# Optimization experiments

Measured on AMD Instinct MI355X. Metric: run time of the kernel, lower is better.

## Reference

```python
import jax, jax.numpy as jnp
import numpy as np

D_MODEL = 1024
NUM_HEAD = 16
HEAD_DIM = D_MODEL // NUM_HEAD
D_OUT = 1024
B, S = 2, 2048


def setup_inputs() -> dict:
    key = jax.random.key(0)
    ks = jax.random.split(key, 11)
    s = 0.02
    return {
        "Q": jax.random.normal(ks[0], (B, S, D_MODEL), jnp.float32),
        "K": jax.random.normal(ks[1], (B, S, D_MODEL), jnp.float32),
        "V": jax.random.normal(ks[2], (B, S, D_MODEL), jnp.float32),
        "Wq": jax.random.normal(ks[3], (D_MODEL, D_MODEL), jnp.float32) * s,
        "bq": jnp.zeros((D_MODEL,), jnp.float32),
        "Wk": jax.random.normal(ks[4], (D_MODEL, D_MODEL), jnp.float32) * s,
        "bk": jnp.zeros((D_MODEL,), jnp.float32),
        "Wv": jax.random.normal(ks[5], (D_MODEL, D_MODEL), jnp.float32) * s,
        "bv": jnp.zeros((D_MODEL,), jnp.float32),
        "Wo": jax.random.normal(ks[6], (D_MODEL, D_OUT), jnp.float32) * s,
        "bo": jnp.zeros((D_OUT,), jnp.float32),
    }


def reference(Q, K, V, Wq, bq, Wk, bk, Wv, bv, Wo, bo):
    T = jnp.asarray(HEAD_DIM, Q.dtype) ** 0.5
    b = Q.shape[0]
    q = (Q @ Wq + bq) / T                      # [B,S,D]
    k = K @ Wk + bk
    v = V @ Wv + bv
    q = q.reshape(b, -1, NUM_HEAD, HEAD_DIM)   # [B,S,H,d]
    k = k.reshape(b, -1, NUM_HEAD, HEAD_DIM)
    v = v.reshape(b, -1, NUM_HEAD, HEAD_DIM)
    scores = jnp.einsum("bqhd,bkhd->bhqk", q, k)
    attn = jax.nn.softmax(scores, axis=-1)
    out = jnp.einsum("bhqk,bkhd->bqhd", attn, v).reshape(b, -1, D_MODEL)
    return out @ Wo + bo
```

## Files before the change

### kernel.cpp

```cpp
#include <hip/hip_runtime.h>
#include <cstdint>
#include <cstddef>

#define D_MODEL 1024
#define HD 64
#define NH 16
#define SEQ 2048
#define NB 2

typedef __attribute__((ext_vector_type(8))) short bf8;
typedef __attribute__((ext_vector_type(8))) unsigned short us8;
typedef __attribute__((ext_vector_type(4))) unsigned short us4;
typedef __attribute__((ext_vector_type(4))) float f4;

__device__ __forceinline__ float bf2f(unsigned short u) {
  union { unsigned int i; float f; } c; c.i = ((unsigned int)u) << 16; return c.f;
}
__device__ __forceinline__ unsigned short f2bf(float x) {
  union { float f; unsigned int i; } c; c.f = x;
  unsigned int r = (c.i + 0x7FFFu + ((c.i >> 16) & 1u)) >> 16;
  return (unsigned short)r;
}
__device__ __forceinline__ unsigned int pkbf(float lo, float hi) {
  unsigned int r;
  asm("v_cvt_pk_bf16_f32 %0, %1, %2" : "=v"(r) : "v"(lo), "v"(hi));
  return r;
}
__device__ __forceinline__ float ex2(float x) {
  float r;
  asm("v_exp_f32 %0, %1" : "=v"(r) : "v"(x));
  return r;
}
__device__ __forceinline__ float max3f(float a, float b, float c) {
  float r;
  asm("v_max3_f32 %0, %1, %2, %3" : "=v"(r) : "v"(a), "v"(b), "v"(c));
  return r;
}
__device__ __forceinline__ f4 mfma16(bf8 a, bf8 b, f4 c) {
  return __builtin_amdgcn_mfma_f32_16x16x32_bf16(a, b, c, 0, 0, 0);
}
__device__ __forceinline__ void gl16(const unsigned short* g, unsigned short* l) {
  __builtin_amdgcn_global_load_lds(
      (const __attribute__((address_space(1))) unsigned int*)g,
      (__attribute__((address_space(3))) unsigned int*)l, 16, 0, 0);
}

#define QSCALE (0.125f * 1.44269504088896f)

__global__ __launch_bounds__(256) void prep_weights(
    const float* __restrict__ Wq, const float* __restrict__ Wk,
    const float* __restrict__ Wv, const float* __restrict__ Wo,
    unsigned short* __restrict__ wthi) {
  int bid = blockIdx.x;
  int mat = bid >> 10, rem = bid & 1023;
  int kt = (rem >> 5) * 32, nt = (rem & 31) * 32;
  const float* W = (mat == 0) ? Wq : (mat == 1) ? Wk : (mat == 2) ? Wv : Wo;
  unsigned short* oh = wthi + ((size_t)mat << 20);
  __shared__ float ls[32][33];
  int i = threadIdx.x >> 5;
  int jj = threadIdx.x & 31;
#pragma unroll
  for (int ii = 0; ii < 4; ++ii) {
    int r = i + ii * 8;
    ls[r][jj] = W[(size_t)(kt + r) * D_MODEL + nt + jj];
  }
  __syncthreads();
#pragma unroll
  for (int ii = 0; ii < 4; ++ii) {
    int r = i + ii * 8;
    float v = ls[jj][r];
    if (mat == 0) v *= QSCALE;
    oh[(size_t)(nt + r) * D_MODEL + kt + jj] = f2bf(v);
  }
}

__global__ __launch_bounds__(256, 3) void proj_gemm(
    const float* __restrict__ Qin, const float* __restrict__ Kin,
    const float* __restrict__ Vin, const unsigned short* __restrict__ wth,
    const float* __restrict__ b0, const float* __restrict__ b1,
    const float* __restrict__ b2,
    unsigned short* __restrict__ qh, unsigned short* __restrict__ kh,
    unsigned short* __restrict__ vt) {
  int wid = (blockIdx.x & 7) * 96 + (blockIdx.x >> 3);
  int z = wid >> 8, rem = wid & 255, bm = rem >> 3, bn = rem & 7;

  const float* A = (z == 0) ? Qin : (z == 1) ? Kin : Vin;
  const unsigned short* Bh = wth + ((size_t)z << 20);
  const float* bias = (z == 0) ? b0 : (z == 1) ? b1 : b2;
  float bsc = (z == 0) ? QSCALE : 1.0f;

  int tid = threadIdx.x, lane = tid & 63, w = tid >> 6;
  int wr = w >> 1, wc = w & 1, l16 = lane & 15, l4 = lane >> 4;

  __shared__ unsigned short As[2][128 * 32];
  __shared__ unsigned short Bsh[2][128 * 32];

  const float* Ab = A + (size_t)(bm * 128) * D_MODEL;
  const unsigned short* Bhb = Bh + (size_t)(bn * 128) * D_MODEL;

  int r0 = tid >> 2, g0 = tid & 3;
  int r1 = (256 + tid) >> 2, g1 = tid & 3;
  int s0 = (r0 ^ (r0 >> 2)) & 3, s1 = (r1 ^ (r1 >> 2)) & 3;
  size_t so0 = (size_t)r0 * D_MODEL + ((g0 ^ s0) * 8);
  size_t so1 = (size_t)r1 * D_MODEL + ((g1 ^ s1) * 8);
  int ld0 = (w * 64) * 8;
  int ld1 = (256 + w * 64) * 8;

  int rr = tid >> 2, c8 = (tid & 3) * 8;
  int adst[2];
#pragma unroll
  for (int p = 0; p < 2; ++p) {
    int row = p * 64 + rr;
    int sw = (row ^ (row >> 2)) & 3;
    adst[p] = row * 32 + (((tid & 3) ^ sw)) * 8;
  }

  int offA[4], offB[4];
#pragma unroll
  for (int m = 0; m < 4; ++m) {
    int row = wr * 64 + m * 16 + l16;
    int sw = (row ^ (row >> 2)) & 3;
    offA[m] = row * 32 + ((l4 ^ sw)) * 8;
  }
#pragma unroll
  for (int n = 0; n < 4; ++n) {
    int row = wc * 64 + n * 16 + l16;
    int sw = (row ^ (row >> 2)) & 3;
    offB[n] = row * 32 + ((l4 ^ sw)) * 8;
  }

  f4 acc[4][4];
  const f4 zf = {0.f, 0.f, 0.f, 0.f};
#pragma unroll
  for (int m = 0; m < 4; ++m)
#pragma unroll
    for (int n = 0; n < 4; ++n) acc[m][n] = zf;

  {
    float4 x[2][2];
#pragma unroll
    for (int p = 0; p < 2; ++p) {
      const float* src = Ab + (size_t)(p * 64 + rr) * D_MODEL + c8;
      x[p][0] = *reinterpret_cast<const float4*>(src);
      x[p][1] = *reinterpret_cast<const float4*>(src + 4);
    }
    gl16(Bhb + so0, &Bsh[0][ld0]);
    gl16(Bhb + so1, &Bsh[0][ld1]);
#pragma unroll
    for (int p = 0; p < 2; ++p) {
      union { us8 v; unsigned u[4]; } hv;
      hv.u[0] = pkbf(x[p][0].x, x[p][0].y); hv.u[1] = pkbf(x[p][0].z, x[p][0].w);
      hv.u[2] = pkbf(x[p][1].x, x[p][1].y); hv.u[3] = pkbf(x[p][1].z, x[p][1].w);
      *reinterpret_cast<us8*>(&As[0][adst[p]]) = hv.v;
    }
  }
  __syncthreads();

  int cur = 0;
  for (int i = 0; i < 32; ++i) {
    float4 nx[2][2];
    if (i < 31) {
      int ktn = (i + 1) * 32;
#pragma unroll
      for (int p = 0; p < 2; ++p) {
        const float* src = Ab + (size_t)(p * 64 + rr) * D_MODEL + ktn + c8;
        nx[p][0] = *reinterpret_cast<const float4*>(src);
        nx[p][1] = *reinterpret_cast<const float4*>(src + 4);
      }
      gl16(Bhb + ktn + so0, &Bsh[cur ^ 1][ld0]);
      gl16(Bhb + ktn + so1, &Bsh[cur ^ 1][ld1]);
    }
    bf8 a[4], bh[4];
#pragma unroll
    for (int m = 0; m < 4; ++m)
      a[m] = *reinterpret_cast<const bf8*>(&As[cur][offA[m]]);
#pragma unroll
    for (int n = 0; n < 4; ++n)
      bh[n] = *reinterpret_cast<const bf8*>(&Bsh[cur][offB[n]]);
#pragma unroll
    for (int m = 0; m < 4; ++m)
#pragma unroll
      for (int n = 0; n < 4; ++n)
        acc[m][n] = mfma16(a[m], bh[n], acc[m][n]);
    if (i < 31) {
#pragma unroll
      for (int p = 0; p < 2; ++p) {
        union { us8 v; unsigned u[4]; } hv;
        hv.u[0] = pkbf(nx[p][0].x, nx[p][0].y); hv.u[1] = pkbf(nx[p][0].z, nx[p][0].w);
        hv.u[2] = pkbf(nx[p][1].x, nx[p][1].y); hv.u[3] = pkbf(nx[p][1].z, nx[p][1].w);
        *reinterpret_cast<us8*>(&As[cur ^ 1][adst[p]]) = hv.v;
      }
    }
    __syncthreads();
    cur ^= 1;
  }

#pragma unroll
  for (int n = 0; n < 4; ++n) {
    int col = bn * 128 + wc * 64 + n * 16 + l16;
    float bb = bias[col] * bsc;
#pragma unroll
    for (int m = 0; m < 4; ++m) {
      int row0 = bm * 128 + wr * 64 + m * 16 + l4 * 4;
      if (z == 0) {
#pragma unroll
        for (int r = 0; r < 4; ++r)
          qh[(size_t)(row0 + r) * D_MODEL + col] = f2bf(acc[m][n][r] + bb);
      } else if (z == 1) {
#pragma unroll
        for (int r = 0; r < 4; ++r)
          kh[(size_t)(row0 + r) * D_MODEL + col] = f2bf(acc[m][n][r] + bb);
      } else {
        int bb2 = row0 >> 11, ss = row0 & (SEQ - 1);
        int hh2 = col >> 6, dd = col & 63;
        union { us4 s; uint2 u; } pk4;
        pk4.u.x = pkbf(acc[m][n][0] + bb, acc[m][n][1] + bb);
        pk4.u.y = pkbf(acc[m][n][2] + bb, acc[m][n][3] + bb);
        *reinterpret_cast<us4*>(vt + ((size_t)(bb2 * NH + hh2) * HD + dd) * SEQ + ss) = pk4.s;
      }
    }
  }
}

__global__ __launch_bounds__(256, 3) void out_gemm(
    const unsigned short* __restrict__ ah, const unsigned short* __restrict__ wth,
    const float* __restrict__ bo, float* __restrict__ o32) {
  int wid = (blockIdx.x & 7) * 64 + (blockIdx.x >> 3);
  int bm = wid >> 4, bn = wid & 15;

  const unsigned short* Bh = wth + ((size_t)3 << 20);
  int tid = threadIdx.x, lane = tid & 63, w = tid >> 6;
  int wr = w >> 1, wc = w & 1, l16 = lane & 15, l4 = lane >> 4;

  __shared__ unsigned short As[2][128 * 32];
  __shared__ unsigned short Bsh[2][64 * 32];

  const unsigned short* Ab = ah + (size_t)(bm * 128) * D_MODEL;
  const unsigned short* Bhb = Bh + (size_t)(bn * 64) * D_MODEL;

  int r0 = tid >> 2, g0 = tid & 3;
  int r1 = (256 + tid) >> 2;
  int s0 = (r0 ^ (r0 >> 2)) & 3, s1 = (r1 ^ (r1 >> 2)) & 3;
  size_t so0 = (size_t)r0 * D_MODEL + ((g0 ^ s0) * 8);
  size_t so1 = (size_t)r1 * D_MODEL + ((g0 ^ s1) * 8);
  int ld0 = (w * 64) * 8;
  int ld1 = (256 + w * 64) * 8;

  int offA[4], offB[2];
#pragma unroll
  for (int m = 0; m < 4; ++m) {
    int row = wr * 64 + m * 16 + l16;
    int sw = (row ^ (row >> 2)) & 3;
    offA[m] = row * 32 + ((l4 ^ sw)) * 8;
  }
#pragma unroll
  for (int n = 0; n < 2; ++n) {
    int row = wc * 32 + n * 16 + l16;
    int sw = (row ^ (row >> 2)) & 3;
    offB[n] = row * 32 + ((l4 ^ sw)) * 8;
  }

  f4 acc[4][2];
  const f4 zf = {0.f, 0.f, 0.f, 0.f};
#pragma unroll
  for (int m = 0; m < 4; ++m)
#pragma unroll
    for (int n = 0; n < 2; ++n) acc[m][n] = zf;

  gl16(Ab + so0, &As[0][ld0]); gl16(Ab + so1, &As[0][ld1]);
  gl16(Bhb + so0, &Bsh[0][ld0]);
  __syncthreads();

  int cur = 0;
  for (int i = 0; i < 32; ++i) {
    if (i < 31) {
      int ktn = (i + 1) * 32;
      gl16(Ab + ktn + so0, &As[cur ^ 1][ld0]); gl16(Ab + ktn + so1, &As[cur ^ 1][ld1]);
      gl16(Bhb + ktn + so0, &Bsh[cur ^ 1][ld0]);
    }
    bf8 a[4], bh[2];
#pragma unroll
    for (int m = 0; m < 4; ++m)
      a[m] = *reinterpret_cast<const bf8*>(&As[cur][offA[m]]);
#pragma unroll
    for (int n = 0; n < 2; ++n)
      bh[n] = *reinterpret_cast<const bf8*>(&Bsh[cur][offB[n]]);
#pragma unroll
    for (int m = 0; m < 4; ++m)
#pragma unroll
      for (int n = 0; n < 2; ++n)
        acc[m][n] = mfma16(a[m], bh[n], acc[m][n]);
    __syncthreads();
    cur ^= 1;
  }

#pragma unroll
  for (int n = 0; n < 2; ++n) {
    int col = bn * 64 + wc * 32 + n * 16 + l16;
    float bb = bo[col];
#pragma unroll
    for (int m = 0; m < 4; ++m) {
      int row0 = bm * 128 + wr * 64 + m * 16 + l4 * 4;
#pragma unroll
      for (int r = 0; r < 4; ++r)
        o32[(size_t)(row0 + r) * D_MODEL + col] = acc[m][n][r] + bb;
    }
  }
}

__global__ __launch_bounds__(256) void attn_kernel(
    const unsigned short* __restrict__ qh, const unsigned short* __restrict__ kh,
    const unsigned short* __restrict__ vt, unsigned short* __restrict__ aout) {
  int orig = blockIdx.x + (blockIdx.y << 4) + (blockIdx.z << 8);
  int swz = ((orig & 7) << 6) + (orig >> 3);
  int qt = swz & 15, h = (swz >> 4) & 15, b = swz >> 8;

  int tid = threadIdx.x;
  int lane = tid & 63, w = tid >> 6;
  int l16 = lane & 15, l4 = lane >> 4;
  int l8r = lane >> 3, l8c = lane & 7;

  __shared__ unsigned short lds[32768];

  const unsigned short* Kh = kh + (size_t)b * SEQ * D_MODEL + h * HD;
  const unsigned short* Vt = vt + (size_t)(b * NH + h) * HD * SEQ;

  bf8 qf[2][2];
#pragma unroll
  for (int m = 0; m < 2; ++m) {
    size_t qo = (size_t)(b * SEQ + qt * 128 + w * 32 + m * 16 + l16) * D_MODEL + h * HD + l4 * 8;
    qf[m][0] = *reinterpret_cast<const bf8*>(qh + qo);
    qf[m][1] = *reinterpret_cast<const bf8*>(qh + qo + 32);
  }
  bf8 ones;
#pragma unroll
  for (int j = 0; j < 8; ++j) ones[j] = (short)0x3F80;

  const f4 zf = {0.f, 0.f, 0.f, 0.f};
  f4 acc[2][4];
  f4 accs[2] = {zf, zf};
  float mr[2] = {0.f, 0.f};
#pragma unroll
  for (int m = 0; m < 2; ++m)
#pragma unroll
    for (int nt = 0; nt < 4; ++nt) acc[m][nt] = zf;

  const int sgr = (l8c ^ l8r) * 8;
  const int swk = l16 & 7;
  const int vsub = ((l4 & 1) << 2);
  const int vrow_in = lane >> 4;

  {
#pragma unroll
    for (int j = 0; j < 4; ++j) {
      int s = w * 4 + j;
      gl16(Kh + (size_t)(8 * s + l8r) * D_MODEL + sgr, &lds[0 + s * 512]);
      int row = 4 * s + vrow_in;
      int g = ((lane & 7) ^ (row & 7)) | (lane & 8);
      gl16(Vt + (size_t)row * SEQ + g * 8, &lds[16384 + s * 512]);
    }
  }
  __syncthreads();

  int cur = 0;
  for (int kt = 0; kt < SEQ / 128; ++kt) {
    if (kt < SEQ / 128 - 1) {
      int k0n = (kt + 1) * 128;
      unsigned short* kd = &lds[(cur ^ 1) * 8192];
      unsigned short* vd = &lds[16384 + (cur ^ 1) * 8192];
#pragma unroll
      for (int j = 0; j < 4; ++j) {
        int s = w * 4 + j;
        gl16(Kh + (size_t)(k0n + 8 * s + l8r) * D_MODEL + sgr, kd + s * 512);
        int row = 4 * s + vrow_in;
        int g = ((lane & 7) ^ (row & 7)) | (lane & 8);
        gl16(Vt + (size_t)row * SEQ + k0n + g * 8, vd + s * 512);
      }
    }
    const unsigned short* khb = &lds[cur * 8192];
    const unsigned short* vlb = &lds[16384 + cur * 8192];

#pragma unroll
    for (int h2 = 0; h2 < 2; ++h2) {
      const unsigned short* khh = khb + h2 * 4096;
      bf8 kb[4][2];
#pragma unroll
      for (int c = 0; c < 4; ++c) {
        int row = c * 16 + l16;
        kb[c][0] = *reinterpret_cast<const bf8*>(&khh[row * 64 + ((l4 ^ swk) * 8)]);
        kb[c][1] = *reinterpret_cast<const bf8*>(&khh[row * 64 + (((4 + l4) ^ swk) * 8)]);
      }
      f4 sc[2][4];
      __builtin_amdgcn_s_setprio(1);
#pragma unroll
      for (int m = 0; m < 2; ++m)
#pragma unroll
        for (int c = 0; c < 4; ++c) {
          f4 sv = zf;
          sv = mfma16(kb[c][0], qf[m][0], sv);
          sv = mfma16(kb[c][1], qf[m][1], sv);
          sc[m][c] = sv;
        }
      __builtin_amdgcn_s_setprio(0);
      uint2 vdr[4][4];
#pragma unroll
      for (int c = 0; c < 4; ++c) {
        int gvc = 2 * c + (l4 >> 1);
        int voff = (((gvc ^ swk) + 8 * h2) << 3) + vsub;
#pragma unroll
        for (int nt = 0; nt < 4; ++nt)
          vdr[c][nt] = *reinterpret_cast<const uint2*>(&vlb[(nt * 16 + l16) * 128 + voff]);
      }
      unsigned Wp[2][4][2];
#pragma unroll
      for (int m = 0; m < 2; ++m) {
        float tc0 = max3f(sc[m][0][0], sc[m][0][1], fmaxf(sc[m][0][2], sc[m][0][3]));
        float tc1 = max3f(sc[m][1][0], sc[m][1][1], fmaxf(sc[m][1][2], sc[m][1][3]));
        float tc2 = max3f(sc[m][2][0], sc[m][2][1], fmaxf(sc[m][2][2], sc[m][2][3]));
        float tc3 = max3f(sc[m][3][0], sc[m][3][1], fmaxf(sc[m][3][2], sc[m][3][3]));
        float tm = max3f(tc0, tc1, fmaxf(tc2, tc3));
        tm = fmaxf(tm, __shfl_xor(tm, 16));
        tm = fmaxf(tm, __shfl_xor(tm, 32));
        if (__any(tm > mr[m] + 8.0f)) {
          float mn = fmaxf(mr[m], tm);
          float al = ex2(mr[m] - mn);
          mr[m] = mn;
          accs[m][0] *= al; accs[m][1] *= al; accs[m][2] *= al; accs[m][3] *= al;
#pragma unroll
          for (int nt = 0; nt < 4; ++nt) {
            acc[m][nt][0] *= al; acc[m][nt][1] *= al;
            acc[m][nt][2] *= al; acc[m][nt][3] *= al;
          }
        }
#pragma unroll
        for (int c = 0; c < 4; ++c) {
          float p0 = ex2(sc[m][c][0] - mr[m]);
          float p1 = ex2(sc[m][c][1] - mr[m]);
          float p2 = ex2(sc[m][c][2] - mr[m]);
          float p3 = ex2(sc[m][c][3] - mr[m]);
          Wp[m][c][0] = pkbf(p0, p1);
          Wp[m][c][1] = pkbf(p2, p3);
        }
      }
      __builtin_amdgcn_s_setprio(1);
#pragma unroll
      for (int cp = 0; cp < 2; ++cp) {
        int c0 = cp * 2, c1 = cp * 2 + 1;
#pragma unroll
        for (int m = 0; m < 2; ++m) {
          union { bf8 v; unsigned u[4]; } pu;
          pu.u[0] = Wp[m][c0][0]; pu.u[1] = Wp[m][c0][1];
          pu.u[2] = Wp[m][c1][0]; pu.u[3] = Wp[m][c1][1];
          accs[m] = mfma16(ones, pu.v, accs[m]);
#pragma unroll
          for (int nt = 0; nt < 4; ++nt) {
            union { bf8 v; unsigned u[4]; } vu;
            vu.u[0] = vdr[c0][nt].x; vu.u[1] = vdr[c0][nt].y;
            vu.u[2] = vdr[c1][nt].x; vu.u[3] = vdr[c1][nt].y;
            acc[m][nt] = mfma16(vu.v, pu.v, acc[m][nt]);
          }
        }
      }
      __builtin_amdgcn_s_setprio(0);
    }
    __syncthreads();
    cur ^= 1;
  }

  float inv[2];
#pragma unroll
  for (int m = 0; m < 2; ++m) inv[m] = 1.0f / accs[m][0];
#pragma unroll
  for (int m = 0; m < 2; ++m) {
    int q = w * 32 + m * 16 + l16;
    int sw = (q & 7) << 3;
#pragma unroll
    for (int nt = 0; nt < 4; ++nt) {
      uint2 pw;
      pw.x = pkbf(acc[m][nt][0] * inv[m], acc[m][nt][1] * inv[m]);
      pw.y = pkbf(acc[m][nt][2] * inv[m], acc[m][nt][3] * inv[m]);
      int d0 = nt * 16 + l4 * 4;
      *reinterpret_cast<uint2*>(&lds[q * 64 + (d0 ^ sw)]) = pw;
    }
  }
  __syncthreads();
  {
    int q = tid >> 1, dh = (tid & 1) * 32, sw = (q & 7) << 3;
    size_t orow = ((size_t)(b * SEQ + qt * 128 + q)) * D_MODEL + h * HD + dh;
#pragma unroll
    for (int j = 0; j < 4; ++j) {
      us8 vv = *reinterpret_cast<const us8*>(&lds[q * 64 + ((dh + j * 8) ^ sw)]);
      *reinterpret_cast<us8*>(&aout[orow + j * 8]) = vv;
    }
  }
}

extern "C" void kernel_launch(void* const* d_in, const int* in_sizes, int n_in,
                              void* d_out, int out_size, void* d_ws, size_t ws_size,
                              hipStream_t stream) {
  const float* Q  = (const float*)d_in[0];
  const float* K  = (const float*)d_in[1];
  const float* V  = (const float*)d_in[2];
  const float* Wq = (const float*)d_in[3];
  const float* bq = (const float*)d_in[4];
  const float* Wk = (const float*)d_in[5];
  const float* bk = (const float*)d_in[6];
  const float* Wv = (const float*)d_in[7];
  const float* bv = (const float*)d_in[8];
  const float* Wo = (const float*)d_in[9];
  const float* bo = (const float*)d_in[10];
  float* out = (float*)d_out;

  unsigned char* ws = (unsigned char*)d_ws;
  const size_t MB = 1024 * 1024;
  unsigned short* wthi = (unsigned short*)(ws);
  unsigned short* qh   = (unsigned short*)(ws + 8 * MB);
  unsigned short* kh   = (unsigned short*)(ws + 16 * MB);
  unsigned short* vt   = (unsigned short*)(ws + 24 * MB);
  unsigned short* ah   = (unsigned short*)(ws + 32 * MB);

  prep_weights<<<dim3(4096, 1, 1), 256, 0, stream>>>(Wq, Wk, Wv, Wo, wthi);
  proj_gemm<<<dim3(768, 1, 1), 256, 0, stream>>>(Q, K, V, wthi,
                                                 bq, bk, bv, qh, kh, vt);
  attn_kernel<<<dim3(16, NH, NB), 256, 0, stream>>>(qh, kh, vt, ah);
  out_gemm<<<dim3(512, 1, 1), 256, 0, stream>>>(ah, wthi, bo, out);
}
```

Measured before the change: 127.6 us.

## Split attention KV across warp pairs with 64-row Q tiles and merge partial softmax

Each attention block now handles 64 query rows instead of 128. Its four waves form two query groups times two KV halves; each wave processes half of every 64-key tile, and the partial softmax state (max, sum, accumulator) is merged through LDS at the end. The grid doubles to 1024 blocks, LDS per block halves, and launch bounds request 4 blocks per CU, all aimed at higher occupancy and better CU fill. The cost is that each K/V tile is reused by fewer query rows, which doubles global K/V traffic, and there is an extra LDS reduction step plus more barriers per key.

Result: no change. 129.5 us (+1.5%).

```diff
diff --git a/kernel.cpp b/kernel.cpp
--- a/kernel.cpp
+++ b/kernel.cpp
@@ -308,19 +308,20 @@
   }
 }
 
-__global__ __launch_bounds__(256) void attn_kernel(
+__global__ __launch_bounds__(256, 4) void attn_kernel(
     const unsigned short* __restrict__ qh, const unsigned short* __restrict__ kh,
     const unsigned short* __restrict__ vt, unsigned short* __restrict__ aout) {
-  int orig = blockIdx.x + (blockIdx.y << 4) + (blockIdx.z << 8);
-  int swz = ((orig & 7) << 6) + (orig >> 3);
-  int qt = swz & 15, h = (swz >> 4) & 15, b = swz >> 8;
+  int orig = blockIdx.x + (blockIdx.y << 5) + (blockIdx.z << 9);
+  int swz = ((orig & 7) << 7) + (orig >> 3);
+  int qt = swz & 31, h = (swz >> 5) & 15, b = swz >> 9;
 
   int tid = threadIdx.x;
   int lane = tid & 63, w = tid >> 6;
+  int wq = w & 1, wk = w >> 1;
   int l16 = lane & 15, l4 = lane >> 4;
   int l8r = lane >> 3, l8c = lane & 7;
 
-  __shared__ unsigned short lds[32768];
+  __shared__ unsigned short lds[16384];
 
   const unsigned short* Kh = kh + (size_t)b * SEQ * D_MODEL + h * HD;
   const unsigned short* Vt = vt + (size_t)(b * NH + h) * HD * SEQ;
@@ -328,7 +329,7 @@
   bf8 qf[2][2];
 #pragma unroll
   for (int m = 0; m < 2; ++m) {
-    size_t qo = (size_t)(b * SEQ + qt * 128 + w * 32 + m * 16 + l16) * D_MODEL + h * HD + l4 * 8;
+    size_t qo = (size_t)(b * SEQ + qt * 64 + wq * 32 + m * 16 + l16) * D_MODEL + h * HD + l4 * 8;
     qf[m][0] = *reinterpret_cast<const bf8*>(qh + qo);
     qf[m][1] = *reinterpret_cast<const bf8*>(qh + qo + 32);
   }
@@ -346,150 +347,150 @@
     for (int nt = 0; nt < 4; ++nt) acc[m][nt] = zf;
 
   const int sgr = (l8c ^ l8r) * 8;
+  const int sl1 = w, sl2 = w + 4;
   const int swk = l16 & 7;
   const int vsub = ((l4 & 1) << 2);
-  const int vrow_in = lane >> 4;
-
-  {
-#pragma unroll
-    for (int j = 0; j < 4; ++j) {
-      int s = w * 4 + j;
-      gl16(Kh + (size_t)(8 * s + l8r) * D_MODEL + sgr, &lds[0 + s * 512]);
-      int row = 4 * s + vrow_in;
-      int g = ((lane & 7) ^ (row & 7)) | (lane & 8);
-      gl16(Vt + (size_t)row * SEQ + g * 8, &lds[16384 + s * 512]);
-    }
-  }
+
+  gl16(Kh + (size_t)(8 * sl1 + l8r) * D_MODEL + sgr, &lds[0 * 4096 + sl1 * 512]);
+  gl16(Kh + (size_t)(8 * sl2 + l8r) * D_MODEL + sgr, &lds[0 * 4096 + sl2 * 512]);
+  gl16(Vt + (size_t)(8 * sl1 + l8r) * SEQ + sgr, &lds[8192 + sl1 * 512]);
+  gl16(Vt + (size_t)(8 * sl2 + l8r) * SEQ + sgr, &lds[8192 + sl2 * 512]);
   __syncthreads();
 
   int cur = 0;
-  for (int kt = 0; kt < SEQ / 128; ++kt) {
-    if (kt < SEQ / 128 - 1) {
-      int k0n = (kt + 1) * 128;
-      unsigned short* kd = &lds[(cur ^ 1) * 8192];
-      unsigned short* vd = &lds[16384 + (cur ^ 1) * 8192];
-#pragma unroll
-      for (int j = 0; j < 4; ++j) {
-        int s = w * 4 + j;
-        gl16(Kh + (size_t)(k0n + 8 * s + l8r) * D_MODEL + sgr, kd + s * 512);
-        int row = 4 * s + vrow_in;
-        int g = ((lane & 7) ^ (row & 7)) | (lane & 8);
-        gl16(Vt + (size_t)row * SEQ + k0n + g * 8, vd + s * 512);
-      }
-    }
-    const unsigned short* khb = &lds[cur * 8192];
-    const unsigned short* vlb = &lds[16384 + cur * 8192];
-
-#pragma unroll
-    for (int h2 = 0; h2 < 2; ++h2) {
-      const unsigned short* khh = khb + h2 * 4096;
-      bf8 kb[4][2];
-#pragma unroll
-      for (int c = 0; c < 4; ++c) {
-        int row = c * 16 + l16;
-        kb[c][0] = *reinterpret_cast<const bf8*>(&khh[row * 64 + ((l4 ^ swk) * 8)]);
-        kb[c][1] = *reinterpret_cast<const bf8*>(&khh[row * 64 + (((4 + l4) ^ swk) * 8)]);
-      }
-      f4 sc[2][4];
-      __builtin_amdgcn_s_setprio(1);
-#pragma unroll
-      for (int m = 0; m < 2; ++m)
-#pragma unroll
-        for (int c = 0; c < 4; ++c) {
-          f4 sv = zf;
-          sv = mfma16(kb[c][0], qf[m][0], sv);
-          sv = mfma16(kb[c][1], qf[m][1], sv);
-          sc[m][c] = sv;
+  for (int kv = 0; kv < SEQ / 64; ++kv) {
+    if (kv < SEQ / 64 - 1) {
+      int k0n = (kv + 1) * 64;
+      unsigned short* kd = &lds[(cur ^ 1) * 4096];
+      unsigned short* vd = &lds[8192 + (cur ^ 1) * 4096];
+      gl16(Kh + (size_t)(k0n + 8 * sl1 + l8r) * D_MODEL + sgr, kd + sl1 * 512);
+      gl16(Kh + (size_t)(k0n + 8 * sl2 + l8r) * D_MODEL + sgr, kd + sl2 * 512);
+      gl16(Vt + (size_t)(8 * sl1 + l8r) * SEQ + k0n + sgr, vd + sl1 * 512);
+      gl16(Vt + (size_t)(8 * sl2 + l8r) * SEQ + k0n + sgr, vd + sl2 * 512);
+    }
+    const unsigned short* khb = &lds[cur * 4096];
+    const unsigned short* vlb = &lds[8192 + cur * 4096];
+
+    bf8 kb[2][2];
+#pragma unroll
+    for (int c = 0; c < 2; ++c) {
+      int row = wk * 32 + c * 16 + l16;
+      kb[c][0] = *reinterpret_cast<const bf8*>(&khb[row * 64 + ((l4 ^ swk) * 8)]);
+      kb[c][1] = *reinterpret_cast<const bf8*>(&khb[row * 64 + (((4 + l4) ^ swk) * 8)]);
+    }
+    f4 sc[2][2];
+    __builtin_amdgcn_s_setprio(1);
+#pragma unroll
+    for (int m = 0; m < 2; ++m)
+#pragma unroll
+      for (int c = 0; c < 2; ++c) {
+        f4 sv = zf;
+        sv = mfma16(kb[c][0], qf[m][0], sv);
+        sv = mfma16(kb[c][1], qf[m][1], sv);
+        sc[m][c] = sv;
+      }
+    __builtin_amdgcn_s_setprio(0);
+    uint2 vdr[2][4];
+#pragma unroll
+    for (int c = 0; c < 2; ++c) {
+      int gvc = 4 * wk + 2 * c + (l4 >> 1);
+      int voff = ((gvc ^ swk) << 3) + vsub;
+#pragma unroll
+      for (int nt = 0; nt < 4; ++nt)
+        vdr[c][nt] = *reinterpret_cast<const uint2*>(&vlb[(nt * 16 + l16) * 64 + voff]);
+    }
+    unsigned Wp[2][2][2];
+#pragma unroll
+    for (int m = 0; m < 2; ++m) {
+      float tc0 = max3f(sc[m][0][0], sc[m][0][1], fmaxf(sc[m][0][2], sc[m][0][3]));
+      float tc1 = max3f(sc[m][1][0], sc[m][1][1], fmaxf(sc[m][1][2], sc[m][1][3]));
+      float tm = fmaxf(tc0, tc1);
+      tm = fmaxf(tm, __shfl_xor(tm, 16));
+      tm = fmaxf(tm, __shfl_xor(tm, 32));
+      if (__any(tm > mr[m] + 8.0f)) {
+        float mn = fmaxf(mr[m], tm);
+        float al = ex2(mr[m] - mn);
+        mr[m] = mn;
+        accs[m][0] *= al; accs[m][1] *= al; accs[m][2] *= al; accs[m][3] *= al;
+#pragma unroll
+        for (int nt = 0; nt < 4; ++nt) {
+          acc[m][nt][0] *= al; acc[m][nt][1] *= al;
+          acc[m][nt][2] *= al; acc[m][nt][3] *= al;
         }
-      __builtin_amdgcn_s_setprio(0);
-      uint2 vdr[4][4];
-#pragma unroll
-      for (int c = 0; c < 4; ++c) {
-        int gvc = 2 * c + (l4 >> 1);
-        int voff = (((gvc ^ swk) + 8 * h2) << 3) + vsub;
-#pragma unroll
-        for (int nt = 0; nt < 4; ++nt)
-          vdr[c][nt] = *reinterpret_cast<const uint2*>(&vlb[(nt * 16 + l16) * 128 + voff]);
-      }
-      unsigned Wp[2][4][2];
-#pragma unroll
-      for (int m = 0; m < 2; ++m) {
-        float tc0 = max3f(sc[m][0][0], sc[m][0][1], fmaxf(sc[m][0][2], sc[m][0][3]));
-        float tc1 = max3f(sc[m][1][0], sc[m][1][1], fmaxf(sc[m][1][2], sc[m][1][3]));
-        float tc2 = max3f(sc[m][2][0], sc[m][2][1], fmaxf(sc[m][2][2], sc[m][2][3]));
-        float tc3 = max3f(sc[m][3][0], sc[m][3][1], fmaxf(sc[m][3][2], sc[m][3][3]));
-        float tm = max3f(tc0, tc1, fmaxf(tc2, tc3));
-        tm = fmaxf(tm, __shfl_xor(tm, 16));
-        tm = fmaxf(tm, __shfl_xor(tm, 32));
-        if (__any(tm > mr[m] + 8.0f)) {
-          float mn = fmaxf(mr[m], tm);
-          float al = ex2(mr[m] - mn);
-          mr[m] = mn;
-          accs[m][0] *= al; accs[m][1] *= al; accs[m][2] *= al; accs[m][3] *= al;
-#pragma unroll
-          for (int nt = 0; nt < 4; ++nt) {
-            acc[m][nt][0] *= al; acc[m][nt][1] *= al;
-            acc[m][nt][2] *= al; acc[m][nt][3] *= al;
-          }
-        }
-#pragma unroll
-        for (int c = 0; c < 4; ++c) {
-          float p0 = ex2(sc[m][c][0] - mr[m]);
-          float p1 = ex2(sc[m][c][1] - mr[m]);
-          float p2 = ex2(sc[m][c][2] - mr[m]);
-          float p3 = ex2(sc[m][c][3] - mr[m]);
-          Wp[m][c][0] = pkbf(p0, p1);
-          Wp[m][c][1] = pkbf(p2, p3);
-        }
-      }
-      __builtin_amdgcn_s_setprio(1);
-#pragma unroll
-      for (int cp = 0; cp < 2; ++cp) {
-        int c0 = cp * 2, c1 = cp * 2 + 1;
-#pragma unroll
-        for (int m = 0; m < 2; ++m) {
-          union { bf8 v; unsigned u[4]; } pu;
-          pu.u[0] = Wp[m][c0][0]; pu.u[1] = Wp[m][c0][1];
-          pu.u[2] = Wp[m][c1][0]; pu.u[3] = Wp[m][c1][1];
-          accs[m] = mfma16(ones, pu.v, accs[m]);
-#pragma unroll
-          for (int nt = 0; nt < 4; ++nt) {
-            union { bf8 v; unsigned u[4]; } vu;
-            vu.u[0] = vdr[c0][nt].x; vu.u[1] = vdr[c0][nt].y;
-            vu.u[2] = vdr[c1][nt].x; vu.u[3] = vdr[c1][nt].y;
-            acc[m][nt] = mfma16(vu.v, pu.v, acc[m][nt]);
-          }
-        }
-      }
-      __builtin_amdgcn_s_setprio(0);
-    }
+      }
+#pragma unroll
+      for (int c = 0; c < 2; ++c) {
+        float p0 = ex2(sc[m][c][0] - mr[m]);
+        float p1 = ex2(sc[m][c][1] - mr[m]);
+        float p2 = ex2(sc[m][c][2] - mr[m]);
+        float p3 = ex2(sc[m][c][3] - mr[m]);
+        Wp[m][c][0] = pkbf(p0, p1);
+        Wp[m][c][1] = pkbf(p2, p3);
+      }
+    }
+    __builtin_amdgcn_s_setprio(1);
+#pragma unroll
+    for (int m = 0; m < 2; ++m) {
+      union { bf8 v; unsigned u[4]; } pu;
+      pu.u[0] = Wp[m][0][0]; pu.u[1] = Wp[m][0][1];
+      pu.u[2] = Wp[m][1][0]; pu.u[3] = Wp[m][1][1];
+      accs[m] = mfma16(ones, pu.v, accs[m]);
+#pragma unroll
+      for (int nt = 0; nt < 4; ++nt) {
+        union { bf8 v; unsigned u[4]; } vu;
+        vu.u[0] = vdr[0][nt].x; vu.u[1] = vdr[0][nt].y;
+        vu.u[2] = vdr[1][nt].x; vu.u[3] = vdr[1][nt].y;
+        acc[m][nt] = mfma16(vu.v, pu.v, acc[m][nt]);
+      }
+    }
+    __builtin_amdgcn_s_setprio(0);
     __syncthreads();
     cur ^= 1;
   }
 
-  float inv[2];
-#pragma unroll
-  for (int m = 0; m < 2; ++m) inv[m] = 1.0f / accs[m][0];
-#pragma unroll
-  for (int m = 0; m < 2; ++m) {
-    int q = w * 32 + m * 16 + l16;
-    int sw = (q & 7) << 3;
-#pragma unroll
-    for (int nt = 0; nt < 4; ++nt) {
-      uint2 pw;
-      pw.x = pkbf(acc[m][nt][0] * inv[m], acc[m][nt][1] * inv[m]);
-      pw.y = pkbf(acc[m][nt][2] * inv[m], acc[m][nt][3] * inv[m]);
-      int d0 = nt * 16 + l4 * 4;
-      *reinterpret_cast<uint2*>(&lds[q * 64 + (d0 ^ sw)]) = pw;
+  float* obuf = reinterpret_cast<float*>(lds);
+  float2* mlb = reinterpret_cast<float2*>(&lds[8704]);
+  unsigned short* obf = &lds[12288];
+  if (wk == 1) {
+#pragma unroll
+    for (int m = 0; m < 2; ++m) {
+      int q = wq * 32 + m * 16 + l16;
+#pragma unroll
+      for (int nt = 0; nt < 4; ++nt)
+        *reinterpret_cast<f4*>(&obuf[q * 68 + nt * 16 + l4 * 4]) = acc[m][nt];
+      if (l4 == 0) mlb[(wq * 2 + m) * 16 + l16] = make_float2(mr[m], accs[m][0]);
+    }
+  }
+  __syncthreads();
+  if (wk == 0) {
+#pragma unroll
+    for (int m = 0; m < 2; ++m) {
+      int q = wq * 32 + m * 16 + l16;
+      float2 p2 = mlb[(wq * 2 + m) * 16 + l16];
+      float M = fmaxf(mr[m], p2.x);
+      float s1 = ex2(mr[m] - M), s2 = ex2(p2.x - M);
+      float inv = 1.0f / (accs[m][0] * s1 + p2.y * s2);
+      int sw = (q & 7) << 3;
+#pragma unroll
+      for (int nt = 0; nt < 4; ++nt) {
+        f4 o2 = *reinterpret_cast<const f4*>(&obuf[q * 68 + nt * 16 + l4 * 4]);
+        uint2 pw;
+        pw.x = pkbf((acc[m][nt][0] * s1 + o2[0] * s2) * inv,
+                    (acc[m][nt][1] * s1 + o2[1] * s2) * inv);
+        pw.y = pkbf((acc[m][nt][2] * s1 + o2[2] * s2) * inv,
+                    (acc[m][nt][3] * s1 + o2[3] * s2) * inv);
+        int d0 = nt * 16 + l4 * 4;
+        *reinterpret_cast<uint2*>(&obf[q * 64 + (d0 ^ sw)]) = pw;
+      }
     }
   }
   __syncthreads();
   {
-    int q = tid >> 1, dh = (tid & 1) * 32, sw = (q & 7) << 3;
-    size_t orow = ((size_t)(b * SEQ + qt * 128 + q)) * D_MODEL + h * HD + dh;
-#pragma unroll
-    for (int j = 0; j < 4; ++j) {
-      us8 vv = *reinterpret_cast<const us8*>(&lds[q * 64 + ((dh + j * 8) ^ sw)]);
+    int q = tid >> 2, dh = (tid & 3) * 16, sw = (q & 7) << 3;
+    size_t orow = ((size_t)(b * SEQ + qt * 64 + q)) * D_MODEL + h * HD + dh;
+#pragma unroll
+    for (int j = 0; j < 2; ++j) {
+      us8 vv = *reinterpret_cast<const us8*>(&obf[q * 64 + ((dh + j * 8) ^ sw)]);
       *reinterpret_cast<us8*>(&aout[orow + j * 8]) = vv;
     }
   }
@@ -522,6 +523,6 @@
   prep_weights<<<dim3(4096, 1, 1), 256, 0, stream>>>(Wq, Wk, Wv, Wo, wthi);
   proj_gemm<<<dim3(768, 1, 1), 256, 0, stream>>>(Q, K, V, wthi,
                                                  bq, bk, bv, qh, kh, vt);
-  attn_kernel<<<dim3(16, NH, NB), 256, 0, stream>>>(qh, kh, vt, ah);
+  attn_kernel<<<dim3(32, NH, NB), 256, 0, stream>>>(qh, kh, vt, ah);
   out_gemm<<<dim3(512, 1, 1), 256, 0, stream>>>(ah, wthi, bo, out);
 }
```
